# Kernel tuning notes

Measured on AMD Instinct MI355X. Metric: run time of the kernel, lower is better.

## Reference

```python
import jax, jax.numpy as jnp
import numpy as np

D_MODEL = 1024
N_HEADS = 16
D_HEAD = D_MODEL // N_HEADS
B, L = 4, 2048
NEG_INF = float('-inf')


def setup_inputs() -> dict:
    key = jax.random.key(0)
    ks = jax.random.split(key, 8)
    x = jax.random.normal(ks[0], (B, L, D_MODEL), dtype=jnp.float32)
    # sorted cumulative event times in hours (~0-2000h span)
    timestamps = jnp.cumsum(jax.random.uniform(ks[1], (B, L), dtype=jnp.float32), axis=-1)
    mask = jnp.ones((B, L), dtype=jnp.float32)
    s = 1.0 / np.sqrt(D_MODEL)
    W_qkv = jax.random.normal(ks[2], (3 * D_MODEL, D_MODEL), dtype=jnp.float32) * s
    b_qkv = jnp.zeros((3 * D_MODEL,), dtype=jnp.float32)
    W_out = jax.random.normal(ks[3], (D_MODEL, D_MODEL), dtype=jnp.float32) * s
    b_out = jnp.zeros((D_MODEL,), dtype=jnp.float32)
    decay_rate = jnp.full((N_HEADS,), 0.01, dtype=jnp.float32)
    return {"x": x, "timestamps": timestamps, "mask": mask,
            "W_qkv": W_qkv, "b_qkv": b_qkv, "W_out": W_out, "b_out": b_out,
            "decay_rate": decay_rate}


def reference(x, timestamps, mask, W_qkv, b_qkv, W_out, b_out, decay_rate):
    Bb, Ll, Dd = x.shape
    H, dh = N_HEADS, D_HEAD
    scale = dh ** (-0.5)
    qkv = x @ W_qkv.T + b_qkv                     # (B,L,3D)
    qkv = qkv.reshape(Bb, Ll, 3, H, dh).transpose(2, 0, 3, 1, 4)  # (3,B,H,L,dh)
    q, k, v = qkv[0], qkv[1], qkv[2]
    attn = jnp.einsum('bhqd,bhkd->bhqk', q, k) * scale
    t_diff = jnp.abs(timestamps[:, :, None] - timestamps[:, None, :])[:, None]  # (B,1,L,L)
    decay = jax.nn.softplus(decay_rate)[None, :, None, None]                    # (1,H,1,1)
    attn = attn - decay * t_diff / 24.0
    causal = jnp.triu(jnp.ones((Ll, Ll), dtype=bool), k=1)        # (L,L) True above diag
    attn = jnp.where(causal[None, None], NEG_INF, attn)
    pad = (mask == 0.0)[:, None, None, :]                         # (B,1,1,L) True=pad key
    attn = jnp.where(pad, NEG_INF, attn)
    attn = jax.nn.softmax(attn, axis=-1)
    out = jnp.einsum('bhqk,bhkd->bhqd', attn, v)                  # (B,H,L,dh)
    out = out.transpose(0, 2, 1, 3).reshape(Bb, Ll, Dd)
    return out @ W_out.T + b_out
```

## Files before the change

### kernel.cpp

```cpp
#include <hip/hip_runtime.h>
#include <stdint.h>
#include <math.h>

#define B_   4
#define L_   2048
#define H_   16
#define DH_  64
#define DM_  1024

typedef __bf16 bf16;
typedef __attribute__((ext_vector_type(8))) __bf16 bf16x8;
typedef __attribute__((ext_vector_type(4))) float f32x4;
typedef __attribute__((ext_vector_type(4))) int i32x4;
typedef __attribute__((ext_vector_type(4))) short s16x4;
typedef unsigned short u16;
typedef unsigned int u32;
typedef __attribute__((ext_vector_type(2))) unsigned int u32x2;
typedef __attribute__((ext_vector_type(4))) unsigned short u16x4;

typedef unsigned int u32g __attribute__((address_space(1)));
typedef unsigned int u32l __attribute__((address_space(3)));

__device__ __forceinline__ u16 f2bf(float f) {
  return __builtin_bit_cast(u16, (bf16)f);
}

__device__ __forceinline__ float exp2_fast(float x) {
  float r; asm("v_exp_f32 %0, %1" : "=v"(r) : "v"(x)); return r;
}

__device__ __forceinline__ void gload16(const void* g, void* l) {
  __builtin_amdgcn_global_load_lds((const u32g*)g, (u32l*)l, 16, 0, 0);
}

__device__ __forceinline__ f32x4 mfma16(s16x4 a, s16x4 b, f32x4 c) {
#if __has_builtin(__builtin_amdgcn_mfma_f32_16x16x16bf16_1k)
  return __builtin_amdgcn_mfma_f32_16x16x16bf16_1k(a, b, c, 0, 0, 0);
#else
  asm volatile("v_mfma_f32_16x16x16_bf16 %0, %1, %2, %0\n\ts_nop 7\n\ts_nop 2"
               : "+v"(c) : "v"(a), "v"(b));
  return c;
#endif
}

#define NX4 2097152
#define NQ4 786432
#define NO4 262144
__global__ __launch_bounds__(256) void cvt3(const float* __restrict__ x,
                                            const float* __restrict__ wq,
                                            const float* __restrict__ wo,
                                            u16* __restrict__ xb, u16* __restrict__ wqb,
                                            u16* __restrict__ wob) {
  int i = blockIdx.x * 256 + threadIdx.x;
  const float* src; u16* dst; int j;
  if (i < NX4)            { src = x;  dst = xb;  j = i; }
  else if (i < NX4 + NQ4) { src = wq; dst = wqb; j = i - NX4; }
  else                    { src = wo; dst = wob; j = i - NX4 - NQ4; }
  f32x4 v = ((const f32x4*)src)[j];
  u16x4 o;
  o[0] = f2bf(v[0]); o[1] = f2bf(v[1]); o[2] = f2bf(v[2]); o[3] = f2bf(v[3]);
  ((u16x4*)dst)[j] = o;
}

__global__ __launch_bounds__(256) void bias_fill(const float* __restrict__ ts,
                                                 const float* __restrict__ msk,
                                                 const float* __restrict__ decay,
                                                 float* __restrict__ Bk) {
  int i = blockIdx.x * 256 + threadIdx.x;
  int bh = i >> 11, l = i & (L_ - 1);
  int b = bh >> 4, h = bh & 15;
  float dc24 = log1pf(__expf(decay[h])) * (1.0f / 24.0f) * 1.44269504f;
  float tv = ts[b * L_ + l], mv = msk[b * L_ + l];
  Bk[i] = (mv != 0.f) ? dc24 * tv : -INFINITY;
}

__global__ __launch_bounds__(512) void gemm_qkv(
    const u16* __restrict__ A, const u16* __restrict__ Bm, const float* __restrict__ bias,
    u16* __restrict__ Qb, u16* __restrict__ Kb, u16* __restrict__ Vt)
{
  __shared__ char smem[135168];
  u16* ltr = (u16*)smem;
  const int K = 1024, nk = 16;

  const int tid = threadIdx.x;
  const int nwg = gridDim.x;
  int idx = blockIdx.x;
  idx = (idx & 7) * (nwg >> 3) + (idx >> 3);
  const int nbx = 12;
  const int bx = idx % nbx, by = idx / nbx;
  const int m0 = by << 8, n0 = bx << 8;

  const int lane = tid & 63, w = tid >> 6;
  const int g = lane >> 4, col = lane & 15;
  const int wr = w >> 2, wc = w & 3;

  f32x4 acc[8][4];
#pragma unroll
  for (int mt = 0; mt < 8; ++mt)
#pragma unroll
    for (int nt = 0; nt < 4; ++nt) {
      acc[mt][nt][0] = 0.f; acc[mt][nt][1] = 0.f;
      acc[mt][nt][2] = 0.f; acc[mt][nt][3] = 0.f;
    }

  auto SA = [&](int kt, int nb, int q) {
    char* dA = smem + (nb << 16);
    int c = (q << 9) + tid;
    int row = c >> 3, cc = c & 7;
    gload16(A + (size_t)(m0 + row) * K + (kt << 6) + ((cc ^ (row & 7)) << 3), dA + c * 16);
  };
  auto SB = [&](int kt, int nb, int q) {
    char* dB = smem + (nb << 16) + 32768;
    int c = (q << 9) + tid;
    int row = c >> 3, cc = c & 7;
    gload16(Bm + (size_t)(n0 + row) * K + (kt << 6) + ((cc ^ (row & 7)) << 3), dB + c * 16);
  };

  SA(0, 0, 0); SA(0, 0, 1); SA(0, 0, 2); SA(0, 0, 3);
  SB(0, 0, 0); SB(0, 0, 1); SB(0, 0, 2); SB(0, 0, 3);
  SA(1, 1, 0); SA(1, 1, 2); SB(1, 1, 0); SB(1, 1, 1); SA(1, 1, 1); SA(1, 1, 3);
  asm volatile("s_waitcnt vmcnt(6)" ::: "memory");
  __builtin_amdgcn_s_barrier();

  for (int t = 0; t < nk; ++t) {
    const char* bufA = smem + ((t & 1) << 16);
    const char* bufB = bufA + 32768;
    const int nbN = (t + 1) & 1;

    auto RDA = [&](int mt, int kk) {
      int row = wr * 128 + mt * 16 + col;
      return *(const bf16x8*)(bufA + row * 128 + ((((kk << 2) + g) ^ (row & 7)) << 4));
    };
    auto RDB = [&](int nt, int kk) {
      int row = wc * 64 + nt * 16 + col;
      return *(const bf16x8*)(bufB + row * 128 + ((((kk << 2) + g) ^ (row & 7)) << 4));
    };

    bf16x8 af[4][2], bfr[4][2];

#pragma unroll
    for (int mi = 0; mi < 4; ++mi) { af[mi][0] = RDA(mi, 0); af[mi][1] = RDA(mi, 1); }
#pragma unroll
    for (int ni = 0; ni < 2; ++ni) { bfr[ni][0] = RDB(ni, 0); bfr[ni][1] = RDB(ni, 1); }
    if (t + 1 < nk) { SB(t + 1, nbN, 2); SB(t + 1, nbN, 3); }
    __builtin_amdgcn_s_barrier();
    asm volatile("s_waitcnt lgkmcnt(0)" ::: "memory");
    __builtin_amdgcn_sched_barrier(0);
    __builtin_amdgcn_s_setprio(1);
#pragma unroll
    for (int mi = 0; mi < 4; ++mi)
#pragma unroll
      for (int ni = 0; ni < 2; ++ni)
#pragma unroll
        for (int kk = 0; kk < 2; ++kk)
          acc[mi][ni] = __builtin_amdgcn_mfma_f32_16x16x32_bf16(af[mi][kk], bfr[ni][kk], acc[mi][ni], 0, 0, 0);
    __builtin_amdgcn_s_setprio(0);
    __builtin_amdgcn_s_barrier();

#pragma unroll
    for (int ni = 2; ni < 4; ++ni) { bfr[ni][0] = RDB(ni, 0); bfr[ni][1] = RDB(ni, 1); }
    if (t + 2 < nk) { SA(t + 2, t & 1, 0); SA(t + 2, t & 1, 2); }
    __builtin_amdgcn_s_barrier();
    asm volatile("s_waitcnt lgkmcnt(0)" ::: "memory");
    __builtin_amdgcn_sched_barrier(0);
    __builtin_amdgcn_s_setprio(1);
#pragma unroll
    for (int mi = 0; mi < 4; ++mi)
#pragma unroll
      for (int ni = 2; ni < 4; ++ni)
#pragma unroll
        for (int kk = 0; kk < 2; ++kk)
          acc[mi][ni] = __builtin_amdgcn_mfma_f32_16x16x32_bf16(af[mi][kk], bfr[ni][kk], acc[mi][ni], 0, 0, 0);
    __builtin_amdgcn_s_setprio(0);
    __builtin_amdgcn_s_barrier();

#pragma unroll
    for (int mi = 0; mi < 4; ++mi) { af[mi][0] = RDA(mi + 4, 0); af[mi][1] = RDA(mi + 4, 1); }
    if (t + 2 < nk) { SB(t + 2, t & 1, 0); SB(t + 2, t & 1, 1); }
    __builtin_amdgcn_s_barrier();
    asm volatile("s_waitcnt lgkmcnt(0)" ::: "memory");
    __builtin_amdgcn_sched_barrier(0);
    __builtin_amdgcn_s_setprio(1);
#pragma unroll
    for (int mi = 0; mi < 4; ++mi)
#pragma unroll
      for (int ni = 2; ni < 4; ++ni)
#pragma unroll
        for (int kk = 0; kk < 2; ++kk)
          acc[mi + 4][ni] = __builtin_amdgcn_mfma_f32_16x16x32_bf16(af[mi][kk], bfr[ni][kk], acc[mi + 4][ni], 0, 0, 0);
    __builtin_amdgcn_s_setprio(0);
    __builtin_amdgcn_s_barrier();

    if (t + 2 < nk) { SA(t + 2, t & 1, 1); SA(t + 2, t & 1, 3); }
    __builtin_amdgcn_s_setprio(1);
#pragma unroll
    for (int mi = 0; mi < 4; ++mi)
#pragma unroll
      for (int ni = 0; ni < 2; ++ni)
#pragma unroll
        for (int kk = 0; kk < 2; ++kk)
          acc[mi + 4][ni] = __builtin_amdgcn_mfma_f32_16x16x32_bf16(af[mi][kk], bfr[ni][kk], acc[mi + 4][ni], 0, 0, 0);
    __builtin_amdgcn_s_setprio(0);
    if (t + 2 < nk) asm volatile("s_waitcnt vmcnt(6)" ::: "memory");
    else            asm volatile("s_waitcnt vmcnt(0)" ::: "memory");
    __builtin_amdgcn_s_barrier();
  }

  const int type = n0 >> 10;
  const float qsc = (type == 0) ? 0.125f * 1.44269504f : 1.0f;
#pragma unroll
  for (int nt = 0; nt < 4; ++nt) {
    int nn = wc * 64 + nt * 16 + col;
    float bv = bias[n0 + nn];
#pragma unroll
    for (int mt = 0; mt < 8; ++mt) {
      int mm = wr * 128 + mt * 16 + g * 4;
#pragma unroll
      for (int r = 0; r < 4; ++r) {
        u16 hv = f2bf((acc[mt][nt][r] + bv) * qsc);
        if (type < 2) ltr[(mm + r) * 264 + nn] = hv;
        else          ltr[nn * 264 + (mm + r)] = hv;
      }
    }
  }
  __syncthreads();
  if (type < 2) {
#pragma unroll
    for (int it = 0; it < 16; ++it) {
      int cid = tid + it * 512;
      int rrow = cid >> 5, cc = cid & 31;
      i32x4 v = *(const i32x4*)((const char*)ltr + rrow * 528 + cc * 16);
      int token = m0 + rrow;
      int bb = token >> 11, ll = token & (L_ - 1);
      int gn = n0 + cc * 8;
      int head = (gn & 1023) >> 6, d = gn & 63;
      u16* dst = (type == 0) ? Qb : Kb;
      *(i32x4*)(dst + ((size_t)((bb * H_ + head) * L_ + ll)) * 64 + d) = v;
    }
  } else {
#pragma unroll
    for (int it = 0; it < 16; ++it) {
      int cid = tid + it * 512;
      int rrow = cid >> 5, cc = cid & 31;
      i32x4 v = *(const i32x4*)((const char*)ltr + rrow * 528 + cc * 16);
      int gn = n0 + rrow;
      int head = (gn & 1023) >> 6, d = gn & 63;
      int token0 = m0 + cc * 8;
      int bb = token0 >> 11, ll = token0 & (L_ - 1);
      *(i32x4*)(Vt + ((size_t)((bb * H_ + head) * DH_ + d)) * L_ + ll) = v;
    }
  }
}

__global__ __launch_bounds__(512) void gemm_bf16(
    const u16* __restrict__ A, const u16* __restrict__ Bm, const float* __restrict__ bias,
    int M, int N, int K, int mode,
    u16* __restrict__ Qb, u16* __restrict__ Kb, u16* __restrict__ Vt, float* __restrict__ Cout)
{
  __shared__ char smem[147456];
  const int tid = threadIdx.x;
  const int nwg = gridDim.x;
  int idx = blockIdx.x;
  idx = (idx & 7) * (nwg >> 3) + (idx >> 3);
  const int nbx = N >> 7;
  const int bx = idx % nbx, by = idx / nbx;
  const int m0 = by << 8, n0 = bx << 7;

  const int lane = tid & 63, w = tid >> 6;
  const int g = lane >> 4, col = lane & 15;
  const int wr = w >> 1, wc = w & 1;

  f32x4 acc[4][4];
#pragma unroll
  for (int mt = 0; mt < 4; ++mt)
#pragma unroll
    for (int nt = 0; nt < 4; ++nt) {
      acc[mt][nt][0] = 0.f; acc[mt][nt][1] = 0.f;
      acc[mt][nt][2] = 0.f; acc[mt][nt][3] = 0.f;
    }

  auto STAGE_A = [&](int kt, int nb, int hh) {
    char* dA = smem + nb * 49152;
    const int k0 = kt << 6;
#pragma unroll
    for (int pp = hh * 2; pp < hh * 2 + 2; ++pp) {
      int c = tid + pp * 512;
      int row = c >> 3, cc = c & 7;
      gload16(A + (size_t)(m0 + row) * K + k0 + ((cc ^ (row & 7)) << 3), dA + c * 16);
    }
  };
  auto STAGE_B = [&](int kt, int nb) {
    char* dB = smem + nb * 49152 + 32768;
    const int k0 = kt << 6;
#pragma unroll
    for (int pp = 0; pp < 2; ++pp) {
      int c = tid + pp * 512;
      int row = c >> 3, cc = c & 7;
      gload16(Bm + (size_t)(n0 + row) * K + k0 + ((cc ^ (row & 7)) << 3), dB + c * 16);
    }
  };

  STAGE_A(0, 0, 0); STAGE_A(0, 0, 1); STAGE_B(0, 0);
  STAGE_A(1, 1, 0); STAGE_A(1, 1, 1); STAGE_B(1, 1);
  asm volatile("s_waitcnt vmcnt(6)" ::: "memory");
  __builtin_amdgcn_s_barrier();

  const int nk = K >> 6;
  for (int t = 0; t < nk; ++t) {
    const char* bufA = smem + (t % 3) * 49152;
    const char* bufB = bufA + 32768;
    const bool pf = (t + 2 < nk);
    const int nb2 = (t + 2) % 3;

    bf16x8 af[4][2], bfr[4][2];
    auto RDA = [&](int mt, int kk) {
      int row = wr * 64 + mt * 16 + col;
      return *(const bf16x8*)(bufA + row * 128 + ((((kk << 2) + g) ^ (row & 7)) << 4));
    };
    auto RDB = [&](int nt, int kk) {
      int row = wc * 64 + nt * 16 + col;
      return *(const bf16x8*)(bufB + row * 128 + ((((kk << 2) + g) ^ (row & 7)) << 4));
    };
    auto QUAD = [&](int qm, int qn) {
      __builtin_amdgcn_s_setprio(1);
#pragma unroll
      for (int mi = 0; mi < 2; ++mi)
#pragma unroll
        for (int ni = 0; ni < 2; ++ni)
#pragma unroll
          for (int kk = 0; kk < 2; ++kk)
            acc[qm * 2 + mi][qn * 2 + ni] = __builtin_amdgcn_mfma_f32_16x16x32_bf16(
                af[qm * 2 + mi][kk], bfr[qn * 2 + ni][kk], acc[qm * 2 + mi][qn * 2 + ni], 0, 0, 0);
      __builtin_amdgcn_s_setprio(0);
    };

#pragma unroll
    for (int mi = 0; mi < 2; ++mi) { af[mi][0] = RDA(mi, 0); af[mi][1] = RDA(mi, 1); }
#pragma unroll
    for (int ni = 0; ni < 2; ++ni) { bfr[ni][0] = RDB(ni, 0); bfr[ni][1] = RDB(ni, 1); }
    if (pf) STAGE_A(t + 2, nb2, 0);
    __builtin_amdgcn_s_barrier();
    asm volatile("s_waitcnt lgkmcnt(0)" ::: "memory");
    __builtin_amdgcn_sched_barrier(0);
    QUAD(0, 0);
    __builtin_amdgcn_s_barrier();

#pragma unroll
    for (int ni = 2; ni < 4; ++ni) { bfr[ni][0] = RDB(ni, 0); bfr[ni][1] = RDB(ni, 1); }
    if (pf) STAGE_A(t + 2, nb2, 1);
    __builtin_amdgcn_s_barrier();
    asm volatile("s_waitcnt lgkmcnt(0)" ::: "memory");
    __builtin_amdgcn_sched_barrier(0);
    QUAD(0, 1);
    __builtin_amdgcn_s_barrier();

#pragma unroll
    for (int mi = 2; mi < 4; ++mi) { af[mi][0] = RDA(mi, 0); af[mi][1] = RDA(mi, 1); }
    if (pf) STAGE_B(t + 2, nb2);
    __builtin_amdgcn_s_barrier();
    asm volatile("s_waitcnt lgkmcnt(0)" ::: "memory");
    __builtin_amdgcn_sched_barrier(0);
    QUAD(1, 1);
    __builtin_amdgcn_s_barrier();

    QUAD(1, 0);
    if (pf)              asm volatile("s_waitcnt vmcnt(6)" ::: "memory");
    else if (t + 1 < nk) asm volatile("s_waitcnt vmcnt(0)" ::: "memory");
    __builtin_amdgcn_s_barrier();
  }

#pragma unroll
  for (int nt = 0; nt < 4; ++nt) {
    int gn = n0 + wc * 64 + nt * 16 + col;
    float bv = bias[gn];
#pragma unroll
    for (int mt = 0; mt < 4; ++mt) {
      int mbase = m0 + wr * 64 + mt * 16 + g * 4;
#pragma unroll
      for (int r = 0; r < 4; ++r)
        Cout[(size_t)(mbase + r) * N + gn] = acc[mt][nt][r] + bv;
    }
  }
}

__global__ __launch_bounds__(512, 2) void attn_fwd(
    const u16* __restrict__ Qb, const u16* __restrict__ Kb, const u16* __restrict__ Vt,
    const float* __restrict__ Bk, u16* __restrict__ AO)
{
  __shared__ u16 lK[3][64 * 64];
  __shared__ u16 lV[3][64 * 64];

  const int phys = blockIdx.x;
  const int xcd = phys & 7, s = phys >> 3;
  const int bh = xcd * 8 + (s >> 3);
  const int pr = s & 7;
  const int qa = pr, qbt = 15 - pr;
  const int b = bh >> 4, h = bh & 15;

  const int tid = threadIdx.x, w = tid >> 6, lane = tid & 63;
  const int g = lane >> 4, q16 = lane & 15;

  const float* Bkb = Bk + (size_t)bh * L_;

  int kcol[2], vcol[4];
#pragma unroll
  for (int kk = 0; kk < 2; ++kk) kcol[kk] = ((kk * 4 + g) ^ (q16 & 7)) << 4;
#pragma unroll
  for (int t = 0; t < 4; ++t)
    vcol[t] = (((2 * t + (g >> 1)) ^ (q16 & 7)) << 4) + (g & 1) * 8;

  const int nkA = (qa + 1) * 2;
  const int nkB = (qbt + 1) * 2;

  auto STAGE = [&](int gst, int nb) {
    const int kt = (gst < nkA) ? gst : gst - nkA;
    const int kg0 = kt * 64;
    const int r8 = tid >> 3, cc = tid & 7;
    gload16(Kb + ((size_t)bh * L_ + kg0 + r8) * 64 + ((cc ^ (r8 & 7)) * 8),
            (char*)lK[nb] + tid * 16);
    gload16(Vt + ((size_t)(bh * 64 + r8)) * L_ + kg0 + ((cc ^ (r8 & 7)) * 8),
            (char*)lV[nb] + tid * 16);
  };

  auto BODY = [&](bf16x8 (&qf)[2], f32x4 (&o)[4], float& l_r, float mn,
                  int qrow, int kg0, int cur) {
    f32x4 sv[4];
#pragma unroll
    for (int t = 0; t < 4; ++t)
      sv[t] = *(const f32x4*)(Bkb + kg0 + t * 16 + g * 4);

    __builtin_amdgcn_s_setprio(1);
#pragma unroll
    for (int t = 0; t < 4; ++t) {
      const char* krow = (const char*)lK[cur] + t * 2048 + q16 * 128;
#pragma unroll
      for (int kk = 0; kk < 2; ++kk) {
        bf16x8 kf = *(const bf16x8*)(krow + kcol[kk]);
        sv[t] = __builtin_amdgcn_mfma_f32_16x16x32_bf16(kf, qf[kk], sv[t], 0, 0, 0);
      }
    }
    __builtin_amdgcn_s_setprio(0);

    if (kg0 + 63 > qrow) {
      const int qg = qrow + q16;
#pragma unroll
      for (int t = 0; t < 4; ++t)
#pragma unroll
        for (int r = 0; r < 4; ++r)
          sv[t][r] = (kg0 + t * 16 + g * 4 + r <= qg) ? sv[t][r] : -INFINITY;
    }

    float rs = 0.f;
#pragma unroll
    for (int t = 0; t < 4; ++t)
#pragma unroll
      for (int r = 0; r < 4; ++r) {
        float pv = exp2_fast(sv[t][r] - mn);
        sv[t][r] = pv;
        rs += pv;
      }
    l_r += rs;

    s16x4 pf[4];
#pragma unroll
    for (int t = 0; t < 4; ++t) {
      s16x4 pp;
      pp[0] = (short)f2bf(sv[t][0]); pp[1] = (short)f2bf(sv[t][1]);
      pp[2] = (short)f2bf(sv[t][2]); pp[3] = (short)f2bf(sv[t][3]);
      pf[t] = pp;
    }

    __builtin_amdgcn_s_setprio(1);
#pragma unroll
    for (int t = 0; t < 4; ++t) {
      const char* vrow = (const char*)lV[cur] + q16 * 128 + vcol[t];
#pragma unroll
      for (int db = 0; db < 4; ++db) {
        s16x4 vf = *(const s16x4*)(vrow + db * 2048);
        o[db] = mfma16(vf, pf[t], o[db]);
      }
    }
    __builtin_amdgcn_s_setprio(0);
  };

  auto EPI = [&](f32x4 (&o)[4], float l_r, int qt) {
    float lt = l_r + __shfl_xor(l_r, 16);
    lt += __shfl_xor(lt, 32);
    float inv = 1.f / lt;
    u16* dst = AO + ((size_t)(b * L_ + qt * 128 + w * 16 + q16)) * DM_ + h * 64 + g * 4;
#pragma unroll
    for (int db = 0; db < 4; ++db) {
      u32x2 pk;
      pk[0] = (u32)f2bf(o[db][0] * inv) | ((u32)f2bf(o[db][1] * inv) << 16);
      pk[1] = (u32)f2bf(o[db][2] * inv) | ((u32)f2bf(o[db][3] * inv) << 16);
      *(u32x2*)(dst + db * 16) = pk;
    }
  };

  STAGE(0, 0);
  STAGE(1, 1);
  asm volatile("s_waitcnt vmcnt(2) lgkmcnt(0)" ::: "memory");
  __builtin_amdgcn_s_barrier();
  __builtin_amdgcn_sched_barrier(0);

  {
    const int qrow = qa * 128 + w * 16;
    const int mkt = (qrow + 79) >> 6;
    const float mn = Bkb[qrow + q16] + 8.f;
    bf16x8 qf[2];
    {
      const u16* Qr = Qb + ((size_t)bh * L_ + qrow + q16) * 64;
      qf[0] = *(const bf16x8*)(Qr + g * 8);
      qf[1] = *(const bf16x8*)(Qr + 32 + g * 8);
    }
    float l_r = 0.f;
    f32x4 o[4];
#pragma unroll
    for (int db = 0; db < 4; ++db) {
      o[db][0] = 0.f; o[db][1] = 0.f; o[db][2] = 0.f; o[db][3] = 0.f;
    }
    for (int st = 0; st < nkA; ++st) {
      const int cur = st % 3;
      STAGE(st + 2, (st + 2) % 3);
      if (st < mkt) BODY(qf, o, l_r, mn, qrow, st * 64, cur);
      asm volatile("s_waitcnt vmcnt(2) lgkmcnt(0)" ::: "memory");
      __builtin_amdgcn_s_barrier();
      __builtin_amdgcn_sched_barrier(0);
    }
    EPI(o, l_r, qa);
  }

  {
    const int qrow = qbt * 128 + w * 16;
    const int mkt = (qrow + 79) >> 6;
    const float mn = Bkb[qrow + q16] + 8.f;
    bf16x8 qf[2];
    {
      const u16* Qr = Qb + ((size_t)bh * L_ + qrow + q16) * 64;
      qf[0] = *(const bf16x8*)(Qr + g * 8);
      qf[1] = *(const bf16x8*)(Qr + 32 + g * 8);
    }
    float l_r = 0.f;
    f32x4 o[4];
#pragma unroll
    for (int db = 0; db < 4; ++db) {
      o[db][0] = 0.f; o[db][1] = 0.f; o[db][2] = 0.f; o[db][3] = 0.f;
    }
    for (int kt = 0; kt < nkB; ++kt) {
      const int gst = nkA + kt;
      const int cur = gst % 3;
      const bool pf = (kt + 2 < nkB);
      if (pf) STAGE(gst + 2, (gst + 2) % 3);
      if (kt < mkt) BODY(qf, o, l_r, mn, qrow, kt * 64, cur);
      if (kt + 1 < nkB) {
        if (pf) asm volatile("s_waitcnt vmcnt(2) lgkmcnt(0)" ::: "memory");
        else    asm volatile("s_waitcnt vmcnt(0) lgkmcnt(0)" ::: "memory");
        __builtin_amdgcn_s_barrier();
        __builtin_amdgcn_sched_barrier(0);
      }
    }
    EPI(o, l_r, qbt);
  }
}

extern "C" void kernel_launch(void* const* d_in, const int* in_sizes, int n_in,
                              void* d_out, int out_size, void* d_ws, size_t ws_size,
                              hipStream_t stream) {
  const float* x    = (const float*)d_in[0];
  const float* ts   = (const float*)d_in[1];
  const float* mk   = (const float*)d_in[2];
  const float* Wqkv = (const float*)d_in[3];
  const float* bqkv = (const float*)d_in[4];
  const float* Wout = (const float*)d_in[5];
  const float* bout = (const float*)d_in[6];
  const float* dec  = (const float*)d_in[7];
  float* out = (float*)d_out;

  char* ws = (char*)d_ws;
  u16* xbf  = (u16*)(ws + 0);
  u16* wqbf = (u16*)(ws + 16777216);
  u16* wobf = (u16*)(ws + 23068672);
  u16* Qb   = (u16*)(ws + 25165824);
  u16* Kb   = (u16*)(ws + 41943040);
  u16* Vt   = (u16*)(ws + 58720256);
  u16* AO   = (u16*)(ws + 75497472);
  float* Bk = (float*)(ws + 92274688);

  cvt3<<<dim3((NX4 + NQ4 + NO4) / 256), 256, 0, stream>>>(x, Wqkv, Wout, xbf, wqbf, wobf);

  bias_fill<<<dim3(64 * 2048 / 256), 256, 0, stream>>>(ts, mk, dec, Bk);

  gemm_qkv<<<dim3(384), 512, 0, stream>>>(xbf, wqbf, bqkv, Qb, Kb, Vt);

  attn_fwd<<<dim3(512), 512, 0, stream>>>(Qb, Kb, Vt, Bk, AO);

  gemm_bf16<<<dim3(256), 512, 0, stream>>>(
      AO, wobf, bout, 8192, 1024, 1024, 1, nullptr, nullptr, nullptr, out);
}
```

Baseline: 174.4 us.

## Software-pipeline QK and PV across key tiles and fuse bias fill into convert

The attention loop is split into a QK/softmax stage and a PV stage. The PV matmul for the previous key tile now runs after the QK matmul of the current tile, so the exp/convert work can overlap with matrix instructions. To keep the previous tile's V buffer valid, prefetch depth drops from two tiles ahead to one, and each iteration waits for all outstanding loads. The separate bias_fill kernel is merged into the conversion kernel, which removes one launch. The shallower prefetch may expose more global-load latency.

```diff
diff --git a/kernel.cpp b/kernel.cpp
--- a/kernel.cpp
+++ b/kernel.cpp
@@ -46,12 +46,26 @@
 #define NX4 2097152
 #define NQ4 786432
 #define NO4 262144
-__global__ __launch_bounds__(256) void cvt3(const float* __restrict__ x,
-                                            const float* __restrict__ wq,
-                                            const float* __restrict__ wo,
-                                            u16* __restrict__ xb, u16* __restrict__ wqb,
-                                            u16* __restrict__ wob) {
+#define NTOT4 (NX4 + NQ4 + NO4)
+__global__ __launch_bounds__(256) void cvt3b(const float* __restrict__ x,
+                                             const float* __restrict__ wq,
+                                             const float* __restrict__ wo,
+                                             u16* __restrict__ xb, u16* __restrict__ wqb,
+                                             u16* __restrict__ wob,
+                                             const float* __restrict__ ts,
+                                             const float* __restrict__ msk,
+                                             const float* __restrict__ decay,
+                                             float* __restrict__ Bk) {
   int i = blockIdx.x * 256 + threadIdx.x;
+  if (i >= NTOT4) {
+    int j = i - NTOT4;
+    int bh = j >> 11, l = j & (L_ - 1);
+    int b = bh >> 4, h = bh & 15;
+    float dc24 = log1pf(__expf(decay[h])) * (1.0f / 24.0f) * 1.44269504f;
+    float tv = ts[b * L_ + l], mv = msk[b * L_ + l];
+    Bk[j] = (mv != 0.f) ? dc24 * tv : -INFINITY;
+    return;
+  }
   const float* src; u16* dst; int j;
   if (i < NX4)            { src = x;  dst = xb;  j = i; }
   else if (i < NX4 + NQ4) { src = wq; dst = wqb; j = i - NX4; }
@@ -60,18 +74,6 @@
   u16x4 o;
   o[0] = f2bf(v[0]); o[1] = f2bf(v[1]); o[2] = f2bf(v[2]); o[3] = f2bf(v[3]);
   ((u16x4*)dst)[j] = o;
-}
-
-__global__ __launch_bounds__(256) void bias_fill(const float* __restrict__ ts,
-                                                 const float* __restrict__ msk,
-                                                 const float* __restrict__ decay,
-                                                 float* __restrict__ Bk) {
-  int i = blockIdx.x * 256 + threadIdx.x;
-  int bh = i >> 11, l = i & (L_ - 1);
-  int b = bh >> 4, h = bh & 15;
-  float dc24 = log1pf(__expf(decay[h])) * (1.0f / 24.0f) * 1.44269504f;
-  float tv = ts[b * L_ + l], mv = msk[b * L_ + l];
-  Bk[i] = (mv != 0.f) ? dc24 * tv : -INFINITY;
 }
 
 __global__ __launch_bounds__(512) void gemm_qkv(
@@ -422,8 +424,8 @@
             (char*)lV[nb] + tid * 16);
   };
 
-  auto BODY = [&](bf16x8 (&qf)[2], f32x4 (&o)[4], float& l_r, float mn,
-                  int qrow, int kg0, int cur) {
+  auto QKBODY = [&](bf16x8 (&qf)[2], float& l_r, float mn,
+                    int qrow, int kg0, int cur, s16x4 (&pf)[4]) {
     f32x4 sv[4];
 #pragma unroll
     for (int t = 0; t < 4; ++t)
@@ -452,28 +454,24 @@
 
     float rs = 0.f;
 #pragma unroll
-    for (int t = 0; t < 4; ++t)
+    for (int t = 0; t < 4; ++t) {
+      s16x4 pp;
 #pragma unroll
       for (int r = 0; r < 4; ++r) {
         float pv = exp2_fast(sv[t][r] - mn);
-        sv[t][r] = pv;
         rs += pv;
+        pp[r] = (short)f2bf(pv);
       }
+      pf[t] = pp;
+    }
     l_r += rs;
-
-    s16x4 pf[4];
+  };
+
+  auto PVBODY = [&](f32x4 (&o)[4], s16x4 (&pf)[4], int vb) {
+    __builtin_amdgcn_s_setprio(1);
 #pragma unroll
     for (int t = 0; t < 4; ++t) {
-      s16x4 pp;
-      pp[0] = (short)f2bf(sv[t][0]); pp[1] = (short)f2bf(sv[t][1]);
-      pp[2] = (short)f2bf(sv[t][2]); pp[3] = (short)f2bf(sv[t][3]);
-      pf[t] = pp;
-    }
-
-    __builtin_amdgcn_s_setprio(1);
-#pragma unroll
-    for (int t = 0; t < 4; ++t) {
-      const char* vrow = (const char*)lV[cur] + q16 * 128 + vcol[t];
+      const char* vrow = (const char*)lV[vb] + q16 * 128 + vcol[t];
 #pragma unroll
       for (int db = 0; db < 4; ++db) {
         s16x4 vf = *(const s16x4*)(vrow + db * 2048);
@@ -498,8 +496,7 @@
   };
 
   STAGE(0, 0);
-  STAGE(1, 1);
-  asm volatile("s_waitcnt vmcnt(2) lgkmcnt(0)" ::: "memory");
+  asm volatile("s_waitcnt vmcnt(0) lgkmcnt(0)" ::: "memory");
   __builtin_amdgcn_s_barrier();
   __builtin_amdgcn_sched_barrier(0);
 
@@ -519,16 +516,30 @@
     for (int db = 0; db < 4; ++db) {
       o[db][0] = 0.f; o[db][1] = 0.f; o[db][2] = 0.f; o[db][3] = 0.f;
     }
+    s16x4 pfP[4];
+    int pvb = 0;
+    bool pvalid = false;
     for (int st = 0; st < nkA; ++st) {
       const int cur = st % 3;
-      STAGE(st + 2, (st + 2) % 3);
-      if (st < mkt) BODY(qf, o, l_r, mn, qrow, st * 64, cur);
-      asm volatile("s_waitcnt vmcnt(2) lgkmcnt(0)" ::: "memory");
+      STAGE(st + 1, (st + 1) % 3);
+      const bool doqk = st < mkt;
+      s16x4 pfC[4];
+      if (doqk) QKBODY(qf, l_r, mn, qrow, st * 64, cur, pfC);
+      if (pvalid) PVBODY(o, pfP, pvb);
+      if (doqk) {
+#pragma unroll
+        for (int t = 0; t < 4; ++t) pfP[t] = pfC[t];
+        pvb = cur;
+      }
+      pvalid = doqk;
+      asm volatile("s_waitcnt vmcnt(0) lgkmcnt(0)" ::: "memory");
       __builtin_amdgcn_s_barrier();
       __builtin_amdgcn_sched_barrier(0);
     }
+    if (pvalid) PVBODY(o, pfP, pvb);
     EPI(o, l_r, qa);
   }
+  __builtin_amdgcn_s_barrier();
 
   {
     const int qrow = qbt * 128 + w * 16;
@@ -546,19 +557,30 @@
     for (int db = 0; db < 4; ++db) {
       o[db][0] = 0.f; o[db][1] = 0.f; o[db][2] = 0.f; o[db][3] = 0.f;
     }
+    s16x4 pfP[4];
+    int pvb = 0;
+    bool pvalid = false;
     for (int kt = 0; kt < nkB; ++kt) {
       const int gst = nkA + kt;
       const int cur = gst % 3;
-      const bool pf = (kt + 2 < nkB);
-      if (pf) STAGE(gst + 2, (gst + 2) % 3);
-      if (kt < mkt) BODY(qf, o, l_r, mn, qrow, kt * 64, cur);
+      if (kt + 1 < nkB) STAGE(gst + 1, (gst + 1) % 3);
+      const bool doqk = kt < mkt;
+      s16x4 pfC[4];
+      if (doqk) QKBODY(qf, l_r, mn, qrow, kt * 64, cur, pfC);
+      if (pvalid) PVBODY(o, pfP, pvb);
+      if (doqk) {
+#pragma unroll
+        for (int t = 0; t < 4; ++t) pfP[t] = pfC[t];
+        pvb = cur;
+      }
+      pvalid = doqk;
       if (kt + 1 < nkB) {
-        if (pf) asm volatile("s_waitcnt vmcnt(2) lgkmcnt(0)" ::: "memory");
-        else    asm volatile("s_waitcnt vmcnt(0) lgkmcnt(0)" ::: "memory");
+        asm volatile("s_waitcnt vmcnt(0) lgkmcnt(0)" ::: "memory");
         __builtin_amdgcn_s_barrier();
         __builtin_amdgcn_sched_barrier(0);
       }
     }
+    if (pvalid) PVBODY(o, pfP, pvb);
     EPI(o, l_r, qbt);
   }
 }
@@ -586,9 +608,8 @@
   u16* AO   = (u16*)(ws + 75497472);
   float* Bk = (float*)(ws + 92274688);
 
-  cvt3<<<dim3((NX4 + NQ4 + NO4) / 256), 256, 0, stream>>>(x, Wqkv, Wout, xbf, wqbf, wobf);
-
-  bias_fill<<<dim3(64 * 2048 / 256), 256, 0, stream>>>(ts, mk, dec, Bk);
+  cvt3b<<<dim3((NTOT4 + 64 * 2048) / 256), 256, 0, stream>>>(
+      x, Wqkv, Wout, xbf, wqbf, wobf, ts, mk, dec, Bk);
 
   gemm_qkv<<<dim3(384), 512, 0, stream>>>(xbf, wqbf, bqkv, Qb, Kb, Vt);
 
```

Result: no change. 171.6 us (median of 3 runs) (-1.6%).
